# Performance work log

Measured on AMD Instinct MI355X. Metric: run time of the kernel, lower is better.

Reference implementation:

```python
import jax, jax.numpy as jnp
import numpy as np

IGNORE_INDEX = -100


def setup_inputs() -> dict:
    key = jax.random.key(0)
    k1, k2, k3 = jax.random.split(key, 3)
    N, H, V = 4096, 2048, 50257
    x = jax.random.normal(k1, (N, H), dtype=jnp.float32)
    weight = jax.random.normal(k2, (V, H), dtype=jnp.float32) * (1.0 / np.sqrt(H))
    y = jax.random.randint(k3, (N,), 0, V, dtype=jnp.int64)
    return {"x": x, "weight": weight, "y": y}


def reference(x, weight, y):
    # Fused linear + cross entropy: logits = x @ W^T, mean NLL over non-ignored tokens.
    logits = jnp.einsum("nh,vh->nv", x, weight)  # [N, V]
    logp = jax.nn.log_softmax(logits, axis=-1)
    mask = (y != IGNORE_INDEX)
    safe_y = jnp.where(mask, y, 0)
    nll = -jnp.take_along_axis(logp, safe_y[:, None], axis=-1)[:, 0]  # [N]
    n_valid = jnp.maximum(jnp.sum(mask), 1)
    loss = jnp.sum(jnp.where(mask, nll, 0.0)) / n_valid.astype(nll.dtype)
    return loss
```

## Files before the change

kernel.cpp:

```cpp
#include <hip/hip_runtime.h>
#include <hip/hip_bf16.h>
#include <math.h>

typedef unsigned char  u8;
typedef unsigned int   u32;
typedef __attribute__((ext_vector_type(8)))  int   int8v;
typedef __attribute__((ext_vector_type(16))) float f32x16;

typedef __attribute__((address_space(3))) void lds_void;
typedef __attribute__((address_space(1))) void gbl_void;

#define IGNORE_INDEX (-100)

__device__ __forceinline__ u8 f32_to_e4m3(float f) {
    union { float f; u32 u; } v; v.f = f;
    u32 s  = (v.u >> 24) & 0x80u;
    u32 au = v.u & 0x7FFFFFFFu;
    float a = __uint_as_float(au);
    if (a >= 448.0f) return (u8)(s | 0x7E);
    int e = (int)(au >> 23) - 127;
    if (e >= -6) {
        u32 m    = au & 0x7FFFFFu;
        u32 keep = m >> 20;
        u32 rest = m & 0xFFFFFu;
        keep += (rest > 0x80000u) || (rest == 0x80000u && (keep & 1u));
        u32 code = ((u32)(e + 7) << 3) + keep;
        if (code > 0x7E) code = 0x7E;
        return (u8)(s | code);
    } else {
        int q = (int)rintf(a * 512.0f);
        return (u8)(s | (u32)q);
    }
}

__global__ __launch_bounds__(256) void cvt_f32_fp8(const float* __restrict__ in,
                                                   u8* __restrict__ out,
                                                   float scale, long n) {
    long i = (long)blockIdx.x * blockDim.x + threadIdx.x;
    long stride = (long)gridDim.x * blockDim.x;
    for (long j = i * 16; j + 15 < n; j += stride * 16) {
        u8 tmp[16];
#pragma unroll
        for (int t = 0; t < 4; ++t) {
            float4 f = *(const float4*)(in + j + t * 4);
            tmp[t * 4 + 0] = f32_to_e4m3(f.x * scale);
            tmp[t * 4 + 1] = f32_to_e4m3(f.y * scale);
            tmp[t * 4 + 2] = f32_to_e4m3(f.z * scale);
            tmp[t * 4 + 3] = f32_to_e4m3(f.w * scale);
        }
        *(int4*)(out + j) = *(const int4*)tmp;
    }
}

__global__ __launch_bounds__(256) void gemm_lse_partial(
    const u8* __restrict__ A8,
    const u8* __restrict__ B8,
    float2* __restrict__ partials,
    int H, int V, int VT)
{
    __shared__ __align__(16) u8 As[16 * 1024];
    __shared__ __align__(16) u8 Bs[16 * 1024];

    const int tid  = threadIdx.x;
    const int w    = tid >> 6;
    const int lane = tid & 63;
    const int wm   = w >> 1, wn = w & 1;
    const int ln32 = lane & 31;
    const int khalf = lane >> 5;

    const int mBase = blockIdx.x * 128;
    const int vTile = blockIdx.y;
    const int vBase = vTile * 128;

    const size_t Hs = (size_t)H;
    const size_t aRow = (size_t)(mBase + w * 32 + ln32);
    int vr = vBase + w * 32 + ln32; if (vr >= V) vr = V - 1;
    const u8* aBase = A8 + aRow * Hs + khalf * 32;
    const u8* bBase = B8 + (size_t)vr * Hs + khalf * 32;
    const int cOff0 = 0, cOff1 = 16, cOff2 = 64, cOff3 = 80;

    f32x16 acc[2][2];
#pragma unroll
    for (int i = 0; i < 2; ++i)
#pragma unroll
        for (int j = 0; j < 2; ++j)
#pragma unroll
            for (int r = 0; r < 16; ++r) acc[i][j][r] = 0.0f;

    const int scaleA = 0x7C7C7C7C;
    const int scaleB = 0x7B7B7B7B;

    const u8* aRd = As + lane * 16;
    const u8* bRd = Bs + lane * 16;

    for (int k0 = 0; k0 < H; k0 += 128) {
        u8* aDst = (u8*)As + w * 4096;
        u8* bDst = (u8*)Bs + w * 4096;
        __builtin_amdgcn_global_load_lds((gbl_void*)(aBase + k0 + cOff0), (lds_void*)(aDst       ), 16, 0, 0);
        __builtin_amdgcn_global_load_lds((gbl_void*)(aBase + k0 + cOff1), (lds_void*)(aDst + 1024), 16, 0, 0);
        __builtin_amdgcn_global_load_lds((gbl_void*)(aBase + k0 + cOff2), (lds_void*)(aDst + 2048), 16, 0, 0);
        __builtin_amdgcn_global_load_lds((gbl_void*)(aBase + k0 + cOff3), (lds_void*)(aDst + 3072), 16, 0, 0);
        __builtin_amdgcn_global_load_lds((gbl_void*)(bBase + k0 + cOff0), (lds_void*)(bDst       ), 16, 0, 0);
        __builtin_amdgcn_global_load_lds((gbl_void*)(bBase + k0 + cOff1), (lds_void*)(bDst + 1024), 16, 0, 0);
        __builtin_amdgcn_global_load_lds((gbl_void*)(bBase + k0 + cOff2), (lds_void*)(bDst + 2048), 16, 0, 0);
        __builtin_amdgcn_global_load_lds((gbl_void*)(bBase + k0 + cOff3), (lds_void*)(bDst + 3072), 16, 0, 0);
        __syncthreads();

#pragma unroll
        for (int ks = 0; ks < 2; ++ks) {
            int8v af[2], bf[2];
#pragma unroll
            for (int i = 0; i < 2; ++i) {
                int sA = ((wm * 2 + i) * 4 + ks * 2) * 1024;
                int4 lo = *(const int4*)(aRd + sA);
                int4 hi = *(const int4*)(aRd + sA + 1024);
                int8v a; a[0]=lo.x; a[1]=lo.y; a[2]=lo.z; a[3]=lo.w;
                         a[4]=hi.x; a[5]=hi.y; a[6]=hi.z; a[7]=hi.w;
                af[i] = a;
                int sB = ((wn * 2 + i) * 4 + ks * 2) * 1024;
                lo = *(const int4*)(bRd + sB);
                hi = *(const int4*)(bRd + sB + 1024);
                int8v b; b[0]=lo.x; b[1]=lo.y; b[2]=lo.z; b[3]=lo.w;
                         b[4]=hi.x; b[5]=hi.y; b[6]=hi.z; b[7]=hi.w;
                bf[i] = b;
            }
#pragma unroll
            for (int i = 0; i < 2; ++i)
#pragma unroll
                for (int j = 0; j < 2; ++j)
                    acc[i][j] = __builtin_amdgcn_mfma_scale_f32_32x32x64_f8f6f4(
                        af[i], bf[j], acc[i][j], 0, 0, 0, scaleA, 0, scaleB);
        }
        __syncthreads();
    }

    bool vj[2];
#pragma unroll
    for (int j = 0; j < 2; ++j)
        vj[j] = (vBase + wn * 64 + j * 32 + ln32) < V;

    float2* red = (float2*)As;

#pragma unroll
    for (int i = 0; i < 2; ++i) {
#pragma unroll
        for (int r = 0; r < 16; ++r) {
            float v0 = vj[0] ? acc[i][0][r] : -INFINITY;
            float v1 = vj[1] ? acc[i][1][r] : -INFINITY;
            float m = fmaxf(v0, v1);
#pragma unroll
            for (int o = 1; o < 32; o <<= 1)
                m = fmaxf(m, __shfl_xor(m, o, 64));
            float s = 0.0f;
            if (vj[0]) s += __expf(acc[i][0][r] - m);
            if (vj[1]) s += __expf(acc[i][1][r] - m);
#pragma unroll
            for (int o = 1; o < 32; o <<= 1)
                s += __shfl_xor(s, o, 64);
            if (ln32 == 0) {
                int row = wm * 64 + i * 32 + (r & 3) + 8 * (r >> 2) + 4 * khalf;
                red[row * 2 + wn] = make_float2(m, s);
            }
        }
    }
    __syncthreads();

    if (tid < 128) {
        float2 p0 = red[tid * 2 + 0];
        float2 p1 = red[tid * 2 + 1];
        float m = fmaxf(p0.x, p1.x);
        float s = p0.y * __expf(p0.x - m) + p1.y * __expf(p1.x - m);
        partials[(size_t)(mBase + tid) * VT + vTile] = make_float2(m, s);
    }
}

__global__ __launch_bounds__(256) void row_final(
    const float* __restrict__ x,
    const float* __restrict__ W,
    const int* __restrict__ y,
    const float2* __restrict__ partials,
    float* __restrict__ nll, float* __restrict__ valid,
    int H, int V, int VT)
{
    const int n = blockIdx.x;
    const int t = threadIdx.x;
    const int yn = y[n];
    const bool ok = (yn != IGNORE_INDEX);

    float dsum = 0.0f;
    if (ok) {
        int cy = yn; if (cy < 0) cy = 0; if (cy >= V) cy = V - 1;
        const float4* xr = (const float4*)(x + (size_t)n * H);
        const float4* wr = (const float4*)(W + (size_t)cy * H);
        int nf4 = H >> 2;
        for (int i = t; i < nf4; i += 256) {
            float4 a = xr[i], b = wr[i];
            dsum += a.x * b.x + a.y * b.y + a.z * b.z + a.w * b.w;
        }
    }

    float m = -INFINITY, s = 0.0f;
    const float2* pr = partials + (size_t)n * VT;
    for (int i = t; i < VT; i += 256) {
        float2 p = pr[i];
        float nm = fmaxf(m, p.x);
        s = s * __expf(m - nm) + p.y * __expf(p.x - nm);
        m = nm;
    }

    __shared__ float rm[256], rs[256], rd[256];
    rm[t] = m; rs[t] = s; rd[t] = dsum;
    __syncthreads();
    for (int o = 128; o > 0; o >>= 1) {
        if (t < o) {
            float m2 = rm[t + o], s2 = rs[t + o];
            float nm = fmaxf(rm[t], m2);
            rs[t] = rs[t] * __expf(rm[t] - nm) + s2 * __expf(m2 - nm);
            rm[t] = nm;
            rd[t] += rd[t + o];
        }
        __syncthreads();
    }
    if (t == 0) {
        float lse = rm[0] + __logf(rs[0]);
        nll[n]   = ok ? (lse - rd[0]) : 0.0f;
        valid[n] = ok ? 1.0f : 0.0f;
    }
}

__global__ __launch_bounds__(1024) void final_loss(
    const float* __restrict__ nll, const float* __restrict__ valid,
    float* __restrict__ out, int n)
{
    __shared__ float ss[1024], sv[1024];
    const int t = threadIdx.x;
    float a = 0.0f, b = 0.0f;
    for (int i = t; i < n; i += 1024) { a += nll[i]; b += valid[i]; }
    ss[t] = a; sv[t] = b;
    __syncthreads();
    for (int o = 512; o > 0; o >>= 1) {
        if (t < o) { ss[t] += ss[t + o]; sv[t] += sv[t + o]; }
        __syncthreads();
    }
    if (t == 0) out[0] = ss[0] / fmaxf(sv[0], 1.0f);
}

extern "C" void kernel_launch(void* const* d_in, const int* in_sizes, int n_in,
                              void* d_out, int out_size, void* d_ws, size_t ws_size,
                              hipStream_t stream) {
    const float* x = (const float*)d_in[0];
    const float* W = (const float*)d_in[1];
    const int*   y = (const int*)d_in[2];

    const long xsz = in_sizes[0];
    const long wsz = in_sizes[1];
    const int  N   = in_sizes[2];
    const int  H   = (int)(xsz / N);
    const int  V   = (int)(wsz / H);
    const int  VT  = (V + 127) / 128;
    const int  MT  = N / 128;

    char* ws = (char*)d_ws;
    size_t off = 0;
    u8* Wf8 = (u8*)(ws + off); off += (size_t)wsz; off = (off + 255) & ~(size_t)255;
    u8* Xf8 = (u8*)(ws + off); off += (size_t)xsz; off = (off + 255) & ~(size_t)255;
    float2* partials = (float2*)(ws + off); off += (size_t)N * VT * sizeof(float2); off = (off + 255) & ~(size_t)255;
    float* nll   = (float*)(ws + off); off += (size_t)N * 4;
    float* valid = (float*)(ws + off); off += (size_t)N * 4;

    int wBlocks = (int)((wsz / 16 + 255) / 256);
    int xBlocks = (int)((xsz / 16 + 255) / 256);
    cvt_f32_fp8<<<wBlocks, 256, 0, stream>>>(W, Wf8, 16.0f, wsz);
    cvt_f32_fp8<<<xBlocks, 256, 0, stream>>>(x, Xf8, 8.0f, xsz);

    dim3 grid(MT, VT);
    gemm_lse_partial<<<grid, 256, 0, stream>>>(Xf8, Wf8, partials, H, V, VT);

    row_final<<<N, 256, 0, stream>>>(x, W, y, partials, nll, valid, H, V, VT);
    final_loss<<<1, 1024, 0, stream>>>(nll, valid, (float*)d_out, N);
}
```

Measured before the change: 1.350 ms.

## Pre-pack FP8 operands into tile-contiguous LDS-ready panels

The FP8 conversion kernels now write X and W as 128-row by 128-column panels laid out exactly as the GEMM's LDS tiles expect, with out-of-range rows zero-padded. The GEMM then streams each k-chunk as one contiguous 16 KB block instead of four strided 16-byte pieces per row. This should give fully coalesced global loads and simpler address arithmetic in the main loop. The cost is an LDS staging pass in the conversion kernels and a padded workspace.

```diff
diff --git a/kernel.cpp b/kernel.cpp
--- a/kernel.cpp
+++ b/kernel.cpp
@@ -33,30 +33,56 @@
     }
 }
 
-__global__ __launch_bounds__(256) void cvt_f32_fp8(const float* __restrict__ in,
-                                                   u8* __restrict__ out,
-                                                   float scale, long n) {
-    long i = (long)blockIdx.x * blockDim.x + threadIdx.x;
-    long stride = (long)gridDim.x * blockDim.x;
-    for (long j = i * 16; j + 15 < n; j += stride * 16) {
+__global__ __launch_bounds__(256) void cvt_pack_fp8(const float* __restrict__ in,
+                                                    u8* __restrict__ out,
+                                                    float scale, int H, int nRows) {
+    __shared__ __align__(16) u8 lds[16384];
+    const int kc    = blockIdx.x;
+    const int panel = blockIdx.y;
+    const int t     = threadIdx.x;
+
+#pragma unroll
+    for (int it = 0; it < 4; ++it) {
+        int u  = it * 256 + t;
+        int r  = u >> 3;
+        int cc = u & 7;
+        int row = panel * 128 + r;
         u8 tmp[16];
-#pragma unroll
-        for (int t = 0; t < 4; ++t) {
-            float4 f = *(const float4*)(in + j + t * 4);
-            tmp[t * 4 + 0] = f32_to_e4m3(f.x * scale);
-            tmp[t * 4 + 1] = f32_to_e4m3(f.y * scale);
-            tmp[t * 4 + 2] = f32_to_e4m3(f.z * scale);
-            tmp[t * 4 + 3] = f32_to_e4m3(f.w * scale);
-        }
-        *(int4*)(out + j) = *(const int4*)tmp;
-    }
+        if (row < nRows) {
+            const float* src = in + (size_t)row * H + kc * 128 + cc * 16;
+#pragma unroll
+            for (int p = 0; p < 4; ++p) {
+                float4 f = *(const float4*)(src + p * 4);
+                tmp[p * 4 + 0] = f32_to_e4m3(f.x * scale);
+                tmp[p * 4 + 1] = f32_to_e4m3(f.y * scale);
+                tmp[p * 4 + 2] = f32_to_e4m3(f.z * scale);
+                tmp[p * 4 + 3] = f32_to_e4m3(f.w * scale);
+            }
+        } else {
+#pragma unroll
+            for (int p = 0; p < 16; ++p) tmp[p] = 0;
+        }
+        int i2 = r >> 5, ln32 = r & 31;
+        int ks = cc >> 2, khalf = (cc >> 1) & 1, h = cc & 1;
+        int s  = i2 * 4 + ks * 2 + h;
+        int lane = khalf * 32 + ln32;
+        *(int4*)(lds + s * 1024 + lane * 16) = *(const int4*)tmp;
+    }
+    __syncthreads();
+
+    u8* dst = out + ((size_t)panel * gridDim.x + kc) * 16384;
+    const int4* l4 = (const int4*)lds;
+    int4* d4 = (int4*)dst;
+#pragma unroll
+    for (int p = 0; p < 4; ++p)
+        d4[p * 256 + t] = l4[p * 256 + t];
 }
 
 __global__ __launch_bounds__(256) void gemm_lse_partial(
-    const u8* __restrict__ A8,
-    const u8* __restrict__ B8,
+    const u8* __restrict__ Ap,
+    const u8* __restrict__ Bp,
     float2* __restrict__ partials,
-    int H, int V, int VT)
+    int KC, int V, int VT)
 {
     __shared__ __align__(16) u8 As[16 * 1024];
     __shared__ __align__(16) u8 Bs[16 * 1024];
@@ -72,13 +98,6 @@
     const int vTile = blockIdx.y;
     const int vBase = vTile * 128;
 
-    const size_t Hs = (size_t)H;
-    const size_t aRow = (size_t)(mBase + w * 32 + ln32);
-    int vr = vBase + w * 32 + ln32; if (vr >= V) vr = V - 1;
-    const u8* aBase = A8 + aRow * Hs + khalf * 32;
-    const u8* bBase = B8 + (size_t)vr * Hs + khalf * 32;
-    const int cOff0 = 0, cOff1 = 16, cOff2 = 64, cOff3 = 80;
-
     f32x16 acc[2][2];
 #pragma unroll
     for (int i = 0; i < 2; ++i)
@@ -90,20 +109,24 @@
     const int scaleA = 0x7C7C7C7C;
     const int scaleB = 0x7B7B7B7B;
 
+    const u8* aSrc = Ap + ((size_t)blockIdx.x * KC) * 16384 + (w * 4096 + lane * 16);
+    const u8* bSrc = Bp + ((size_t)vTile      * KC) * 16384 + (w * 4096 + lane * 16);
+    u8* aDst = (u8*)As + w * 4096;
+    u8* bDst = (u8*)Bs + w * 4096;
+
     const u8* aRd = As + lane * 16;
     const u8* bRd = Bs + lane * 16;
 
-    for (int k0 = 0; k0 < H; k0 += 128) {
-        u8* aDst = (u8*)As + w * 4096;
-        u8* bDst = (u8*)Bs + w * 4096;
-        __builtin_amdgcn_global_load_lds((gbl_void*)(aBase + k0 + cOff0), (lds_void*)(aDst       ), 16, 0, 0);
-        __builtin_amdgcn_global_load_lds((gbl_void*)(aBase + k0 + cOff1), (lds_void*)(aDst + 1024), 16, 0, 0);
-        __builtin_amdgcn_global_load_lds((gbl_void*)(aBase + k0 + cOff2), (lds_void*)(aDst + 2048), 16, 0, 0);
-        __builtin_amdgcn_global_load_lds((gbl_void*)(aBase + k0 + cOff3), (lds_void*)(aDst + 3072), 16, 0, 0);
-        __builtin_amdgcn_global_load_lds((gbl_void*)(bBase + k0 + cOff0), (lds_void*)(bDst       ), 16, 0, 0);
-        __builtin_amdgcn_global_load_lds((gbl_void*)(bBase + k0 + cOff1), (lds_void*)(bDst + 1024), 16, 0, 0);
-        __builtin_amdgcn_global_load_lds((gbl_void*)(bBase + k0 + cOff2), (lds_void*)(bDst + 2048), 16, 0, 0);
-        __builtin_amdgcn_global_load_lds((gbl_void*)(bBase + k0 + cOff3), (lds_void*)(bDst + 3072), 16, 0, 0);
+    for (int kc = 0; kc < KC; ++kc) {
+        __builtin_amdgcn_global_load_lds((gbl_void*)(aSrc       ), (lds_void*)(aDst       ), 16, 0, 0);
+        __builtin_amdgcn_global_load_lds((gbl_void*)(aSrc + 1024), (lds_void*)(aDst + 1024), 16, 0, 0);
+        __builtin_amdgcn_global_load_lds((gbl_void*)(aSrc + 2048), (lds_void*)(aDst + 2048), 16, 0, 0);
+        __builtin_amdgcn_global_load_lds((gbl_void*)(aSrc + 3072), (lds_void*)(aDst + 3072), 16, 0, 0);
+        __builtin_amdgcn_global_load_lds((gbl_void*)(bSrc       ), (lds_void*)(bDst       ), 16, 0, 0);
+        __builtin_amdgcn_global_load_lds((gbl_void*)(bSrc + 1024), (lds_void*)(bDst + 1024), 16, 0, 0);
+        __builtin_amdgcn_global_load_lds((gbl_void*)(bSrc + 2048), (lds_void*)(bDst + 2048), 16, 0, 0);
+        __builtin_amdgcn_global_load_lds((gbl_void*)(bSrc + 3072), (lds_void*)(bDst + 3072), 16, 0, 0);
+        aSrc += 16384; bSrc += 16384;
         __syncthreads();
 
 #pragma unroll
@@ -259,22 +282,21 @@
     const int  V   = (int)(wsz / H);
     const int  VT  = (V + 127) / 128;
     const int  MT  = N / 128;
+    const int  KC  = H / 128;
 
     char* ws = (char*)d_ws;
     size_t off = 0;
-    u8* Wf8 = (u8*)(ws + off); off += (size_t)wsz; off = (off + 255) & ~(size_t)255;
-    u8* Xf8 = (u8*)(ws + off); off += (size_t)xsz; off = (off + 255) & ~(size_t)255;
+    u8* Wp = (u8*)(ws + off); off += (size_t)VT * KC * 16384; off = (off + 255) & ~(size_t)255;
+    u8* Xp = (u8*)(ws + off); off += (size_t)MT * KC * 16384; off = (off + 255) & ~(size_t)255;
     float2* partials = (float2*)(ws + off); off += (size_t)N * VT * sizeof(float2); off = (off + 255) & ~(size_t)255;
     float* nll   = (float*)(ws + off); off += (size_t)N * 4;
     float* valid = (float*)(ws + off); off += (size_t)N * 4;
 
-    int wBlocks = (int)((wsz / 16 + 255) / 256);
-    int xBlocks = (int)((xsz / 16 + 255) / 256);
-    cvt_f32_fp8<<<wBlocks, 256, 0, stream>>>(W, Wf8, 16.0f, wsz);
-    cvt_f32_fp8<<<xBlocks, 256, 0, stream>>>(x, Xf8, 8.0f, xsz);
+    cvt_pack_fp8<<<dim3(KC, VT), 256, 0, stream>>>(W, Wp, 16.0f, H, V);
+    cvt_pack_fp8<<<dim3(KC, MT), 256, 0, stream>>>(x, Xp, 8.0f, H, N);
 
     dim3 grid(MT, VT);
-    gemm_lse_partial<<<grid, 256, 0, stream>>>(Xf8, Wf8, partials, H, V, VT);
+    gemm_lse_partial<<<grid, 256, 0, stream>>>(Xp, Wp, partials, KC, V, VT);
 
     row_final<<<N, 256, 0, stream>>>(x, W, y, partials, nll, valid, H, V, VT);
     final_loss<<<1, 1024, 0, stream>>>(nll, valid, (float*)d_out, N);
```

Result: faster. 1.229 ms (-8.9%).
